# Optimization experiments

Hardware: AMD Instinct MI355X
Metric: run time of the kernel (lower is better)

Reference implementation:

```python
import jax, jax.numpy as jnp
import numpy as np

H = 4  # num_heads
EPS = 1e-5


def setup_inputs() -> dict:
    key = jax.random.key(0)
    ks = jax.random.split(key, 12)
    N, C, E = 4096, 128, 131072
    x = jax.random.normal(ks[0], (N, C), dtype=jnp.float32)
    edge_index = jax.random.randint(ks[1], (2, E), 0, N, dtype=jnp.int64)
    # guarantee every row has at least one neighbor (self-loops) to avoid NaN softmax rows
    loops = jnp.arange(N, dtype=jnp.int64)
    edge_index = edge_index.at[0, :N].set(loops).at[1, :N].set(loops)
    s = 1.0 / np.sqrt(C)
    def lin(k):
        kw, kb = jax.random.split(k)
        return (jax.random.uniform(kw, (C, C), jnp.float32, -s, s),
                jax.random.uniform(kb, (C,), jnp.float32, -s, s))
    wq, bq = lin(ks[2]); wk, bk = lin(ks[3]); wv, bv = lin(ks[4]); wo, bo = lin(ks[5])
    gamma = jnp.ones((C,), jnp.float32)
    beta = jnp.zeros((C,), jnp.float32)
    return {"x": x, "edge_index": edge_index, "wq": wq, "bq": bq, "wk": wk, "bk": bk,
            "wv": wv, "bv": bv, "wo": wo, "bo": bo, "gamma": gamma, "beta": beta}


def reference(x, edge_index, wq, bq, wk, bk, wv, bv, wo, bo, gamma, beta):
    N, C = x.shape
    D = C // H
    q = (x @ wq.T + bq).reshape(N, H, D)
    k = (x @ wk.T + bk).reshape(N, H, D)
    v = (x @ wv.T + bv).reshape(N, H, D)
    scores = jnp.einsum('nhd,mhd->nhm', q, k) / jnp.sqrt(jnp.float32(D))  # [N,H,N]
    row, col = edge_index
    mask = jnp.zeros((N, N), jnp.float32).at[row, col].set(1.0)
    scores = jnp.where(mask[:, None, :] == 0, -jnp.inf, scores)
    attn = jax.nn.softmax(scores, axis=-1)  # dropout is identity in eval
    out = jnp.einsum('nhm,mhd->nhd', attn, v).reshape(N, C)
    out = out @ wo.T + bo
    y = x + out
    mu = jnp.mean(y, axis=-1, keepdims=True)
    var = jnp.var(y, axis=-1, keepdims=True)
    return (y - mu) / jnp.sqrt(var + EPS) * gamma + beta
```

## Files before the change

kernel.cpp:

```cpp
#include <hip/hip_runtime.h>

typedef unsigned long long u64;
typedef unsigned short u16;
typedef __attribute__((ext_vector_type(8))) short short8;
typedef __attribute__((ext_vector_type(4))) float f32x4;

#define C_DIM 128
#define MAXN 128

__device__ inline u16 bf16_rn(float f) {
    unsigned u = __float_as_uint(f);
    u += 0x7FFF + ((u >> 16) & 1);
    return (u16)(u >> 16);
}
__device__ inline float bf16_tof(u16 h) { return __uint_as_float(((unsigned)h) << 16); }

__global__ __launch_bounds__(256) void prep_kernel(
    const int* __restrict__ ei, int E, u64* __restrict__ bm, int wpr,
    const float* __restrict__ x, u16* __restrict__ xh, u16* __restrict__ xl, int xq,
    const float* __restrict__ wq, const float* __restrict__ wk,
    const float* __restrict__ wv, const float* __restrict__ wo,
    u16* __restrict__ wH, u16* __restrict__ wL)
{
    int tid = blockIdx.x * 256 + threadIdx.x;
    if (tid < E) {
        int r = ei[tid], c = ei[E + tid];
        atomicOr(&bm[(size_t)r * wpr + (c >> 6)], 1ull << (c & 63));
    }
    if (tid < 4 * C_DIM * C_DIM) {
        int s = tid >> 14, i = tid & 16383;
        const float* W = (s == 0) ? wq : (s == 1) ? wk : (s == 2) ? wv : wo;
        float f = W[i];
        u16 h = bf16_rn(f);
        wH[tid] = h;
        wL[tid] = bf16_rn(f - bf16_tof(h));
    }
    if (tid < xq) {
        float4 xv = ((const float4*)x)[tid];
        ushort4 h, l;
        h.x = bf16_rn(xv.x); l.x = bf16_rn(xv.x - bf16_tof(h.x));
        h.y = bf16_rn(xv.y); l.y = bf16_rn(xv.y - bf16_tof(h.y));
        h.z = bf16_rn(xv.z); l.z = bf16_rn(xv.z - bf16_tof(h.z));
        h.w = bf16_rn(xv.w); l.w = bf16_rn(xv.w - bf16_tof(h.w));
        ((ushort4*)xh)[tid] = h;
        ((ushort4*)xl)[tid] = l;
    }
}

__global__ __launch_bounds__(256) void qkv_mfma_kernel(
    const u16* __restrict__ xh, const u16* __restrict__ xl,
    const u16* __restrict__ wH, const u16* __restrict__ wL,
    const float* __restrict__ bq, const float* __restrict__ bk, const float* __restrict__ bv,
    float* __restrict__ qo, float* __restrict__ ko, float* __restrict__ vo, int nrg)
{
    int bid = blockIdx.x;
    int s = bid / nrg;
    int rg = bid % nrg;
    int r0 = rg * 16;
    int w  = threadIdx.x >> 6;
    int l  = threadIdx.x & 63;
    int j0 = w * 32;
    int lr = l & 15;
    int kg = l >> 4;

    const u16* xhp = xh + (size_t)(r0 + lr) * C_DIM + kg * 8;
    const u16* xlp = xl + (size_t)(r0 + lr) * C_DIM + kg * 8;
    const u16* wh  = wH + (size_t)s * C_DIM * C_DIM;
    const u16* wl  = wL + (size_t)s * C_DIM * C_DIM;
    const u16* w0h = wh + (size_t)(j0 + lr) * C_DIM + kg * 8;
    const u16* w0l = wl + (size_t)(j0 + lr) * C_DIM + kg * 8;
    const u16* w1h = w0h + 16 * C_DIM;
    const u16* w1l = w0l + 16 * C_DIM;
    const float* B = (s == 0) ? bq : (s == 1) ? bk : bv;
    float*       O = (s == 0) ? qo : (s == 1) ? ko : vo;
    float fin = (s == 0) ? 0.17677669529663687f : 1.0f;

    float b0 = B[j0 + lr], b1 = B[j0 + 16 + lr];
    f32x4 acc0 = {b0, b0, b0, b0};
    f32x4 acc1 = {b1, b1, b1, b1};

    #pragma unroll
    for (int kk = 0; kk < C_DIM; kk += 32) {
        short8 ah  = *(const short8*)(xhp + kk);
        short8 al  = *(const short8*)(xlp + kk);
        short8 bh0 = *(const short8*)(w0h + kk);
        short8 bl0 = *(const short8*)(w0l + kk);
        short8 bh1 = *(const short8*)(w1h + kk);
        short8 bl1 = *(const short8*)(w1l + kk);
        acc0 = __builtin_amdgcn_mfma_f32_16x16x32_bf16(ah, bh0, acc0, 0, 0, 0);
        acc0 = __builtin_amdgcn_mfma_f32_16x16x32_bf16(ah, bl0, acc0, 0, 0, 0);
        acc0 = __builtin_amdgcn_mfma_f32_16x16x32_bf16(al, bh0, acc0, 0, 0, 0);
        acc1 = __builtin_amdgcn_mfma_f32_16x16x32_bf16(ah, bh1, acc1, 0, 0, 0);
        acc1 = __builtin_amdgcn_mfma_f32_16x16x32_bf16(ah, bl1, acc1, 0, 0, 0);
        acc1 = __builtin_amdgcn_mfma_f32_16x16x32_bf16(al, bh1, acc1, 0, 0, 0);
    }
    size_t ob = (size_t)(r0 + kg * 4) * C_DIM;
    #pragma unroll
    for (int i = 0; i < 4; ++i) {
        O[ob + (size_t)i * C_DIM + j0 + lr]      = acc0[i] * fin;
        O[ob + (size_t)i * C_DIM + j0 + 16 + lr] = acc1[i] * fin;
    }
}

__global__ __launch_bounds__(512, 4) void attn_kernel(
    const float* __restrict__ q, const float* __restrict__ k,
    const float* __restrict__ v, const u64* __restrict__ bm, int wpr,
    u16* __restrict__ aoh, u16* __restrict__ aol)
{
    __shared__ int   lm[8][MAXN];
    __shared__ float ls[8][4][MAXN];
    int t = threadIdx.x;
    int wave = t >> 6, lane = t & 63;
    int n = blockIdx.x * 8 + wave;

    u64 bits = bm[(size_t)n * wpr + lane];
    int pc = __popcll(bits);
    int incl = pc;
    #pragma unroll
    for (int off = 1; off < 64; off <<= 1) {
        int tv = __shfl_up(incl, off);
        if (lane >= off) incl += tv;
    }
    int cnt = __shfl(incl, 63);
    int pos = incl - pc;
    u64 bb = bits;
    while (bb) {
        int b = __builtin_ctzll(bb);
        bb &= bb - 1;
        if (pos < MAXN) lm[wave][pos] = (lane << 6) + b;
        ++pos;
    }
    if (cnt > MAXN) cnt = MAXN;

    {
        int nb = lane & 15, hh = lane >> 4;
        const float* qp = q + (size_t)n * C_DIM + hh * 32;
        float4 qf[8];
        #pragma unroll
        for (int u = 0; u < 8; ++u) qf[u] = *(const float4*)(qp + u * 4);
        for (int j0 = 0; j0 < cnt; j0 += 32) {
            int ja = j0 + nb, jb = j0 + 16 + nb;
            int ma = lm[wave][ja < cnt ? ja : 0];
            int mb = lm[wave][jb < cnt ? jb : 0];
            const float* ka = k + (size_t)ma * C_DIM + hh * 32;
            const float* kb = k + (size_t)mb * C_DIM + hh * 32;
            float4 A[8], B[8];
            #pragma unroll
            for (int u = 0; u < 8; ++u) {
                A[u] = *(const float4*)(ka + u * 4);
                B[u] = *(const float4*)(kb + u * 4);
            }
            float sa = 0.f, sb = 0.f;
            #pragma unroll
            for (int u = 0; u < 8; ++u) {
                sa += qf[u].x * A[u].x + qf[u].y * A[u].y
                    + qf[u].z * A[u].z + qf[u].w * A[u].w;
                sb += qf[u].x * B[u].x + qf[u].y * B[u].y
                    + qf[u].z * B[u].z + qf[u].w * B[u].w;
            }
            if (ja < cnt) ls[wave][hh][ja] = sa;
            if (jb < cnt) ls[wave][hh][jb] = sb;
        }
    }
    float2 vbuf[32];
    #pragma unroll
    for (int u = 0; u < 32; ++u) {
        int m = lm[wave][u < cnt ? u : 0];
        vbuf[u] = *(const float2*)(v + (size_t)m * C_DIM + 2 * lane);
    }
    int g = lane >> 4, li = lane & 15;
    float mx = -1e30f;
    for (int jj = li; jj < cnt; jj += 16) mx = fmaxf(mx, ls[wave][g][jj]);
    #pragma unroll
    for (int off = 8; off; off >>= 1) mx = fmaxf(mx, __shfl_xor(mx, off));
    float sum = 0.f;
    for (int jj = li; jj < cnt; jj += 16) {
        float e = __expf(ls[wave][g][jj] - mx);
        ls[wave][g][jj] = e;
        sum += e;
    }
    #pragma unroll
    for (int off = 8; off; off >>= 1) sum += __shfl_xor(sum, off);
    float sinv = 1.0f / sum;
    float2 acc = {0.f, 0.f};
    for (int j0 = 0; j0 < cnt; j0 += 32) {
        if (j0) {
            #pragma unroll
            for (int u = 0; u < 32; ++u) {
                int jj = j0 + u;
                int m = lm[wave][jj < cnt ? jj : 0];
                vbuf[u] = *(const float2*)(v + (size_t)m * C_DIM + 2 * lane);
            }
        }
        int cc = cnt - j0; if (cc > 32) cc = 32;
        #pragma unroll
        for (int u = 0; u < 32; ++u) {
            if (u < cc) {
                float e = ls[wave][g][j0 + u];
                acc.x += e * vbuf[u].x;
                acc.y += e * vbuf[u].y;
            }
        }
    }
    float f0 = acc.x * sinv, f1 = acc.y * sinv;
    ushort2 ho, lo;
    ho.x = bf16_rn(f0); lo.x = bf16_rn(f0 - bf16_tof(ho.x));
    ho.y = bf16_rn(f1); lo.y = bf16_rn(f1 - bf16_tof(ho.y));
    *(ushort2*)(aoh + (size_t)n * C_DIM + 2 * lane) = ho;
    *(ushort2*)(aol + (size_t)n * C_DIM + 2 * lane) = lo;
}

__global__ __launch_bounds__(256) void oln_kernel(
    const u16* __restrict__ aoh, const u16* __restrict__ aol,
    const u16* __restrict__ woh, const u16* __restrict__ wol,
    const float* __restrict__ bo, const float* __restrict__ x,
    const float* __restrict__ gamma, const float* __restrict__ beta,
    float* __restrict__ out)
{
    __shared__ float ys[8 * 132];
    int r0 = blockIdx.x * 8;
    int w  = threadIdx.x >> 6;
    int l  = threadIdx.x & 63;
    int j0 = w * 32;
    int lr = l & 15;
    int kg = l >> 4;
    int ar = lr & 7;

    const u16* ahp = aoh + (size_t)(r0 + ar) * C_DIM + kg * 8;
    const u16* alp = aol + (size_t)(r0 + ar) * C_DIM + kg * 8;
    const u16* w0h = woh + (size_t)(j0 + lr) * C_DIM + kg * 8;
    const u16* w0l = wol + (size_t)(j0 + lr) * C_DIM + kg * 8;
    const u16* w1h = w0h + 16 * C_DIM;
    const u16* w1l = w0l + 16 * C_DIM;

    float b0 = bo[j0 + lr], b1 = bo[j0 + 16 + lr];
    f32x4 acc0 = {b0, b0, b0, b0};
    f32x4 acc1 = {b1, b1, b1, b1};

    #pragma unroll
    for (int kk = 0; kk < C_DIM; kk += 32) {
        short8 ah  = *(const short8*)(ahp + kk);
        short8 al  = *(const short8*)(alp + kk);
        short8 bh0 = *(const short8*)(w0h + kk);
        short8 bl0 = *(const short8*)(w0l + kk);
        short8 bh1 = *(const short8*)(w1h + kk);
        short8 bl1 = *(const short8*)(w1l + kk);
        acc0 = __builtin_amdgcn_mfma_f32_16x16x32_bf16(ah, bh0, acc0, 0, 0, 0);
        acc0 = __builtin_amdgcn_mfma_f32_16x16x32_bf16(ah, bl0, acc0, 0, 0, 0);
        acc0 = __builtin_amdgcn_mfma_f32_16x16x32_bf16(al, bh0, acc0, 0, 0, 0);
        acc1 = __builtin_amdgcn_mfma_f32_16x16x32_bf16(ah, bh1, acc1, 0, 0, 0);
        acc1 = __builtin_amdgcn_mfma_f32_16x16x32_bf16(ah, bl1, acc1, 0, 0, 0);
        acc1 = __builtin_amdgcn_mfma_f32_16x16x32_bf16(al, bh1, acc1, 0, 0, 0);
    }
    #pragma unroll
    for (int i = 0; i < 4; ++i) {
        int rr = kg * 4 + i;
        if (rr < 8) {
            float y0 = acc0[i] + x[(size_t)(r0 + rr) * C_DIM + j0 + lr];
            float y1 = acc1[i] + x[(size_t)(r0 + rr) * C_DIM + j0 + 16 + lr];
            ys[rr * 132 + j0 + lr]      = y0;
            ys[rr * 132 + j0 + 16 + lr] = y1;
        }
    }
    __syncthreads();
    if (threadIdx.x < 128) {
        int rr = threadIdx.x >> 4;
        int c0 = (threadIdx.x & 15) * 8;
        float yv[8];
        float s = 0.f, s2 = 0.f;
        #pragma unroll
        for (int u = 0; u < 8; ++u) {
            yv[u] = ys[rr * 132 + c0 + u];
            s += yv[u]; s2 += yv[u] * yv[u];
        }
        #pragma unroll
        for (int off = 8; off; off >>= 1) {
            s  += __shfl_xor(s, off);
            s2 += __shfl_xor(s2, off);
        }
        float mu = s * (1.0f / 128.0f);
        float var = s2 * (1.0f / 128.0f) - mu * mu;
        float rstd = rsqrtf(var + 1e-5f);
        size_t o = (size_t)(r0 + rr) * C_DIM + c0;
        #pragma unroll
        for (int u = 0; u < 8; ++u)
            out[o + u] = (yv[u] - mu) * rstd * gamma[c0 + u] + beta[c0 + u];
    }
}

extern "C" void kernel_launch(void* const* d_in, const int* in_sizes, int n_in,
                              void* d_out, int out_size, void* d_ws, size_t ws_size,
                              hipStream_t stream)
{
    const float* x     = (const float*)d_in[0];
    const int*   ei    = (const int*)d_in[1];
    const float* wq    = (const float*)d_in[2];
    const float* bq    = (const float*)d_in[3];
    const float* wk    = (const float*)d_in[4];
    const float* bk    = (const float*)d_in[5];
    const float* wv    = (const float*)d_in[6];
    const float* bv    = (const float*)d_in[7];
    const float* wo    = (const float*)d_in[8];
    const float* bo    = (const float*)d_in[9];
    const float* gamma = (const float*)d_in[10];
    const float* beta  = (const float*)d_in[11];
    float* out = (float*)d_out;

    int N = in_sizes[0] / C_DIM;
    int E = in_sizes[1] / 2;
    int wpr = N >> 6;

    size_t MB = 1 << 20;
    char* base = (char*)d_ws;
    float* q   = (float*)(base + 0 * MB);
    float* k   = (float*)(base + 2 * MB);
    float* v   = (float*)(base + 4 * MB);
    u64*   bm  = (u64*)(base + 6 * MB);
    u16*   xh  = (u16*)(base + 8 * MB);
    u16*   xl  = (u16*)(base + 9 * MB);
    u16*   wH  = (u16*)(base + 10 * MB);
    u16*   wL  = (u16*)(base + 10 * MB + 512 * 1024);
    u16*   aoh = (u16*)(base + 11 * MB);
    u16*   aol = (u16*)(base + 12 * MB);

    hipMemsetAsync(bm, 0, (size_t)N * wpr * sizeof(u64), stream);

    int xq = N * C_DIM / 4;
    int nwork = (E > xq) ? E : xq;
    prep_kernel<<<(nwork + 255) / 256, 256, 0, stream>>>(
        ei, E, bm, wpr, x, xh, xl, xq, wq, wk, wv, wo, wH, wL);

    int nrg = N / 16;
    qkv_mfma_kernel<<<3 * nrg, 256, 0, stream>>>(
        xh, xl, wH, wL, bq, bk, bv, q, k, v, nrg);

    attn_kernel<<<N / 8, 512, 0, stream>>>(q, k, v, bm, wpr, aoh, aol);

    oln_kernel<<<N / 8, 256, 0, stream>>>(
        aoh, aol, wH + 3 * C_DIM * C_DIM, wL + 3 * C_DIM * C_DIM,
        bo, x, gamma, beta, out);
}
```

Measured before the change: 126.5 us.

## Fuse prep into QKV GEMM with inline bf16 split, widen oln tiles

Removes the separate prep kernel. The QKV kernel now builds the edge bitmask and splits fp32 x and weights into bf16 hi/lo on the fly inside the MFMA loop, and the output projection splits wo inline too. The oln kernel now processes 16 rows per block, so no MFMA rows are wasted. The attention kernel skips loading the second K half and out-of-range V rows when there are fewer neighbors. This saves a launch and the round trips through intermediate buffers, at the cost of repeated conversion arithmetic and fp32 global loads inside the GEMMs.

```diff
diff --git a/kernel.cpp b/kernel.cpp
--- a/kernel.cpp
+++ b/kernel.cpp
@@ -15,45 +15,33 @@
 }
 __device__ inline float bf16_tof(u16 h) { return __uint_as_float(((unsigned)h) << 16); }
 
-__global__ __launch_bounds__(256) void prep_kernel(
+__device__ inline void split8(float4 a, float4 b, short8* h, short8* l) {
+    float f[8] = {a.x, a.y, a.z, a.w, b.x, b.y, b.z, b.w};
+    short8 hh, ll;
+    #pragma unroll
+    for (int i = 0; i < 8; ++i) {
+        u16 hu = bf16_rn(f[i]);
+        hh[i] = (short)hu;
+        ll[i] = (short)bf16_rn(f[i] - bf16_tof(hu));
+    }
+    *h = hh; *l = ll;
+}
+
+__global__ __launch_bounds__(256) void qkv_fused_kernel(
     const int* __restrict__ ei, int E, u64* __restrict__ bm, int wpr,
-    const float* __restrict__ x, u16* __restrict__ xh, u16* __restrict__ xl, int xq,
-    const float* __restrict__ wq, const float* __restrict__ wk,
-    const float* __restrict__ wv, const float* __restrict__ wo,
-    u16* __restrict__ wH, u16* __restrict__ wL)
+    const float* __restrict__ x,
+    const float* __restrict__ wq, const float* __restrict__ bq,
+    const float* __restrict__ wk, const float* __restrict__ bk,
+    const float* __restrict__ wv, const float* __restrict__ bv,
+    float* __restrict__ qo, float* __restrict__ ko, float* __restrict__ vo, int nrg)
 {
-    int tid = blockIdx.x * 256 + threadIdx.x;
+    int bid = blockIdx.x;
+    int tid = bid * 256 + threadIdx.x;
     if (tid < E) {
         int r = ei[tid], c = ei[E + tid];
         atomicOr(&bm[(size_t)r * wpr + (c >> 6)], 1ull << (c & 63));
     }
-    if (tid < 4 * C_DIM * C_DIM) {
-        int s = tid >> 14, i = tid & 16383;
-        const float* W = (s == 0) ? wq : (s == 1) ? wk : (s == 2) ? wv : wo;
-        float f = W[i];
-        u16 h = bf16_rn(f);
-        wH[tid] = h;
-        wL[tid] = bf16_rn(f - bf16_tof(h));
-    }
-    if (tid < xq) {
-        float4 xv = ((const float4*)x)[tid];
-        ushort4 h, l;
-        h.x = bf16_rn(xv.x); l.x = bf16_rn(xv.x - bf16_tof(h.x));
-        h.y = bf16_rn(xv.y); l.y = bf16_rn(xv.y - bf16_tof(h.y));
-        h.z = bf16_rn(xv.z); l.z = bf16_rn(xv.z - bf16_tof(h.z));
-        h.w = bf16_rn(xv.w); l.w = bf16_rn(xv.w - bf16_tof(h.w));
-        ((ushort4*)xh)[tid] = h;
-        ((ushort4*)xl)[tid] = l;
-    }
-}
-
-__global__ __launch_bounds__(256) void qkv_mfma_kernel(
-    const u16* __restrict__ xh, const u16* __restrict__ xl,
-    const u16* __restrict__ wH, const u16* __restrict__ wL,
-    const float* __restrict__ bq, const float* __restrict__ bk, const float* __restrict__ bv,
-    float* __restrict__ qo, float* __restrict__ ko, float* __restrict__ vo, int nrg)
-{
-    int bid = blockIdx.x;
+
     int s = bid / nrg;
     int rg = bid % nrg;
     int r0 = rg * 16;
@@ -63,30 +51,25 @@
     int lr = l & 15;
     int kg = l >> 4;
 
-    const u16* xhp = xh + (size_t)(r0 + lr) * C_DIM + kg * 8;
-    const u16* xlp = xl + (size_t)(r0 + lr) * C_DIM + kg * 8;
-    const u16* wh  = wH + (size_t)s * C_DIM * C_DIM;
-    const u16* wl  = wL + (size_t)s * C_DIM * C_DIM;
-    const u16* w0h = wh + (size_t)(j0 + lr) * C_DIM + kg * 8;
-    const u16* w0l = wl + (size_t)(j0 + lr) * C_DIM + kg * 8;
-    const u16* w1h = w0h + 16 * C_DIM;
-    const u16* w1l = w0l + 16 * C_DIM;
+    const float* W = (s == 0) ? wq : (s == 1) ? wk : wv;
     const float* B = (s == 0) ? bq : (s == 1) ? bk : bv;
     float*       O = (s == 0) ? qo : (s == 1) ? ko : vo;
     float fin = (s == 0) ? 0.17677669529663687f : 1.0f;
 
+    const float* xp  = x + (size_t)(r0 + lr) * C_DIM + kg * 8;
+    const float* w0p = W + (size_t)(j0 + lr) * C_DIM + kg * 8;
+    const float* w1p = w0p + 16 * C_DIM;
+
     float b0 = B[j0 + lr], b1 = B[j0 + 16 + lr];
     f32x4 acc0 = {b0, b0, b0, b0};
     f32x4 acc1 = {b1, b1, b1, b1};
 
     #pragma unroll
     for (int kk = 0; kk < C_DIM; kk += 32) {
-        short8 ah  = *(const short8*)(xhp + kk);
-        short8 al  = *(const short8*)(xlp + kk);
-        short8 bh0 = *(const short8*)(w0h + kk);
-        short8 bl0 = *(const short8*)(w0l + kk);
-        short8 bh1 = *(const short8*)(w1h + kk);
-        short8 bl1 = *(const short8*)(w1l + kk);
+        short8 ah, al, bh0, bl0, bh1, bl1;
+        split8(*(const float4*)(xp + kk),  *(const float4*)(xp + kk + 4),  &ah,  &al);
+        split8(*(const float4*)(w0p + kk), *(const float4*)(w0p + kk + 4), &bh0, &bl0);
+        split8(*(const float4*)(w1p + kk), *(const float4*)(w1p + kk + 4), &bh1, &bl1);
         acc0 = __builtin_amdgcn_mfma_f32_16x16x32_bf16(ah, bh0, acc0, 0, 0, 0);
         acc0 = __builtin_amdgcn_mfma_f32_16x16x32_bf16(ah, bl0, acc0, 0, 0, 0);
         acc0 = __builtin_amdgcn_mfma_f32_16x16x32_bf16(al, bh0, acc0, 0, 0, 0);
@@ -121,7 +104,7 @@
         int tv = __shfl_up(incl, off);
         if (lane >= off) incl += tv;
     }
-    int cnt = __shfl(incl, 63);
+    int cnt = __builtin_amdgcn_readfirstlane(__shfl(incl, 63));
     int pos = incl - pc;
     u64 bb = bits;
     while (bb) {
@@ -140,33 +123,41 @@
         for (int u = 0; u < 8; ++u) qf[u] = *(const float4*)(qp + u * 4);
         for (int j0 = 0; j0 < cnt; j0 += 32) {
             int ja = j0 + nb, jb = j0 + 16 + nb;
+            bool doB = (j0 + 16) < cnt;
             int ma = lm[wave][ja < cnt ? ja : 0];
-            int mb = lm[wave][jb < cnt ? jb : 0];
             const float* ka = k + (size_t)ma * C_DIM + hh * 32;
-            const float* kb = k + (size_t)mb * C_DIM + hh * 32;
             float4 A[8], B[8];
             #pragma unroll
-            for (int u = 0; u < 8; ++u) {
-                A[u] = *(const float4*)(ka + u * 4);
-                B[u] = *(const float4*)(kb + u * 4);
+            for (int u = 0; u < 8; ++u) A[u] = *(const float4*)(ka + u * 4);
+            if (doB) {
+                int mb = lm[wave][jb < cnt ? jb : 0];
+                const float* kb = k + (size_t)mb * C_DIM + hh * 32;
+                #pragma unroll
+                for (int u = 0; u < 8; ++u) B[u] = *(const float4*)(kb + u * 4);
             }
-            float sa = 0.f, sb = 0.f;
+            float sa = 0.f;
             #pragma unroll
-            for (int u = 0; u < 8; ++u) {
+            for (int u = 0; u < 8; ++u)
                 sa += qf[u].x * A[u].x + qf[u].y * A[u].y
                     + qf[u].z * A[u].z + qf[u].w * A[u].w;
-                sb += qf[u].x * B[u].x + qf[u].y * B[u].y
-                    + qf[u].z * B[u].z + qf[u].w * B[u].w;
+            if (ja < cnt) ls[wave][hh][ja] = sa;
+            if (doB) {
+                float sb = 0.f;
+                #pragma unroll
+                for (int u = 0; u < 8; ++u)
+                    sb += qf[u].x * B[u].x + qf[u].y * B[u].y
+                        + qf[u].z * B[u].z + qf[u].w * B[u].w;
+                if (jb < cnt) ls[wave][hh][jb] = sb;
             }
-            if (ja < cnt) ls[wave][hh][ja] = sa;
-            if (jb < cnt) ls[wave][hh][jb] = sb;
         }
     }
     float2 vbuf[32];
     #pragma unroll
     for (int u = 0; u < 32; ++u) {
-        int m = lm[wave][u < cnt ? u : 0];
-        vbuf[u] = *(const float2*)(v + (size_t)m * C_DIM + 2 * lane);
+        if (u < cnt) {
+            int m = lm[wave][u];
+            vbuf[u] = *(const float2*)(v + (size_t)m * C_DIM + 2 * lane);
+        }
     }
     int g = lane >> 4, li = lane & 15;
     float mx = -1e30f;
@@ -187,9 +178,10 @@
         if (j0) {
             #pragma unroll
             for (int u = 0; u < 32; ++u) {
-                int jj = j0 + u;
-                int m = lm[wave][jj < cnt ? jj : 0];
-                vbuf[u] = *(const float2*)(v + (size_t)m * C_DIM + 2 * lane);
+                if (j0 + u < cnt) {
+                    int m = lm[wave][j0 + u];
+                    vbuf[u] = *(const float2*)(v + (size_t)m * C_DIM + 2 * lane);
+                }
             }
         }
         int cc = cnt - j0; if (cc > 32) cc = 32;
@@ -212,26 +204,23 @@
 
 __global__ __launch_bounds__(256) void oln_kernel(
     const u16* __restrict__ aoh, const u16* __restrict__ aol,
-    const u16* __restrict__ woh, const u16* __restrict__ wol,
-    const float* __restrict__ bo, const float* __restrict__ x,
+    const float* __restrict__ wo, const float* __restrict__ bo,
+    const float* __restrict__ x,
     const float* __restrict__ gamma, const float* __restrict__ beta,
     float* __restrict__ out)
 {
-    __shared__ float ys[8 * 132];
-    int r0 = blockIdx.x * 8;
+    __shared__ float ys[16 * 132];
+    int r0 = blockIdx.x * 16;
     int w  = threadIdx.x >> 6;
     int l  = threadIdx.x & 63;
     int j0 = w * 32;
     int lr = l & 15;
     int kg = l >> 4;
-    int ar = lr & 7;
-
-    const u16* ahp = aoh + (size_t)(r0 + ar) * C_DIM + kg * 8;
-    const u16* alp = aol + (size_t)(r0 + ar) * C_DIM + kg * 8;
-    const u16* w0h = woh + (size_t)(j0 + lr) * C_DIM + kg * 8;
-    const u16* w0l = wol + (size_t)(j0 + lr) * C_DIM + kg * 8;
-    const u16* w1h = w0h + 16 * C_DIM;
-    const u16* w1l = w0l + 16 * C_DIM;
+
+    const u16* ahp = aoh + (size_t)(r0 + lr) * C_DIM + kg * 8;
+    const u16* alp = aol + (size_t)(r0 + lr) * C_DIM + kg * 8;
+    const float* w0p = wo + (size_t)(j0 + lr) * C_DIM + kg * 8;
+    const float* w1p = w0p + 16 * C_DIM;
 
     float b0 = bo[j0 + lr], b1 = bo[j0 + 16 + lr];
     f32x4 acc0 = {b0, b0, b0, b0};
@@ -241,10 +230,9 @@
     for (int kk = 0; kk < C_DIM; kk += 32) {
         short8 ah  = *(const short8*)(ahp + kk);
         short8 al  = *(const short8*)(alp + kk);
-        short8 bh0 = *(const short8*)(w0h + kk);
-        short8 bl0 = *(const short8*)(w0l + kk);
-        short8 bh1 = *(const short8*)(w1h + kk);
-        short8 bl1 = *(const short8*)(w1l + kk);
+        short8 bh0, bl0, bh1, bl1;
+        split8(*(const float4*)(w0p + kk), *(const float4*)(w0p + kk + 4), &bh0, &bl0);
+        split8(*(const float4*)(w1p + kk), *(const float4*)(w1p + kk + 4), &bh1, &bl1);
         acc0 = __builtin_amdgcn_mfma_f32_16x16x32_bf16(ah, bh0, acc0, 0, 0, 0);
         acc0 = __builtin_amdgcn_mfma_f32_16x16x32_bf16(ah, bl0, acc0, 0, 0, 0);
         acc0 = __builtin_amdgcn_mfma_f32_16x16x32_bf16(al, bh0, acc0, 0, 0, 0);
@@ -255,15 +243,13 @@
     #pragma unroll
     for (int i = 0; i < 4; ++i) {
         int rr = kg * 4 + i;
-        if (rr < 8) {
-            float y0 = acc0[i] + x[(size_t)(r0 + rr) * C_DIM + j0 + lr];
-            float y1 = acc1[i] + x[(size_t)(r0 + rr) * C_DIM + j0 + 16 + lr];
-            ys[rr * 132 + j0 + lr]      = y0;
-            ys[rr * 132 + j0 + 16 + lr] = y1;
-        }
+        float y0 = acc0[i] + x[(size_t)(r0 + rr) * C_DIM + j0 + lr];
+        float y1 = acc1[i] + x[(size_t)(r0 + rr) * C_DIM + j0 + 16 + lr];
+        ys[rr * 132 + j0 + lr]      = y0;
+        ys[rr * 132 + j0 + 16 + lr] = y1;
     }
     __syncthreads();
-    if (threadIdx.x < 128) {
+    {
         int rr = threadIdx.x >> 4;
         int c0 = (threadIdx.x & 15) * 8;
         float yv[8];
@@ -316,27 +302,17 @@
     float* k   = (float*)(base + 2 * MB);
     float* v   = (float*)(base + 4 * MB);
     u64*   bm  = (u64*)(base + 6 * MB);
-    u16*   xh  = (u16*)(base + 8 * MB);
-    u16*   xl  = (u16*)(base + 9 * MB);
-    u16*   wH  = (u16*)(base + 10 * MB);
-    u16*   wL  = (u16*)(base + 10 * MB + 512 * 1024);
-    u16*   aoh = (u16*)(base + 11 * MB);
-    u16*   aol = (u16*)(base + 12 * MB);
+    u16*   aoh = (u16*)(base + 8 * MB);
+    u16*   aol = (u16*)(base + 9 * MB);
 
     hipMemsetAsync(bm, 0, (size_t)N * wpr * sizeof(u64), stream);
 
-    int xq = N * C_DIM / 4;
-    int nwork = (E > xq) ? E : xq;
-    prep_kernel<<<(nwork + 255) / 256, 256, 0, stream>>>(
-        ei, E, bm, wpr, x, xh, xl, xq, wq, wk, wv, wo, wH, wL);
-
     int nrg = N / 16;
-    qkv_mfma_kernel<<<3 * nrg, 256, 0, stream>>>(
-        xh, xl, wH, wL, bq, bk, bv, q, k, v, nrg);
+    qkv_fused_kernel<<<3 * nrg, 256, 0, stream>>>(
+        ei, E, bm, wpr, x, wq, bq, wk, bk, wv, bv, q, k, v, nrg);
 
     attn_kernel<<<N / 8, 512, 0, stream>>>(q, k, v, bm, wpr, aoh, aol);
 
-    oln_kernel<<<N / 8, 256, 0, stream>>>(
-        aoh, aol, wH + 3 * C_DIM * C_DIM, wL + 3 * C_DIM * C_DIM,
-        bo, x, gamma, beta, out);
-}
+    oln_kernel<<<N / 16, 256, 0, stream>>>(
+        aoh, aol, wo, bo, x, gamma, beta, out);
+}
```

Measured after the change: 139.1 us. 10.0% more time.
